# Kernel tuning notes

Hardware: AMD Instinct MI355X
Metric: run time of the kernel (lower is better)

## Reference

```python
import jax, jax.numpy as jnp
import numpy as np

P_DROP = 0.5

def _dropout(x, key):
    keep = jax.random.bernoulli(key, 1.0 - P_DROP, x.shape)
    return jnp.where(keep, x / (1.0 - P_DROP), 0.0)

def _sage_mean_agg(src, dst, feat_src, h_self, n_dst, key):
    # SAGEMeanAgg: dropout both inputs, copy_src gather, segment mean, add, relu
    k1, k2 = jax.random.split(key)
    feat_src = _dropout(feat_src, k1)
    h_self = _dropout(h_self, k2)
    msg = feat_src[src]                                   # [E, d] gather
    summ = jax.ops.segment_sum(msg, dst, num_segments=n_dst)
    deg = jax.ops.segment_sum(jnp.ones((dst.shape[0],), msg.dtype), dst, num_segments=n_dst)
    neigh = jnp.where(deg[:, None] > 0, summ / jnp.maximum(deg, 1.0)[:, None], 0.0)
    return jax.nn.relu(neigh + h_self)

def setup_inputs() -> dict:
    key = jax.random.key(0)
    ks = jax.random.split(key, 12)
    N_total, d_in, d_hid, d_out = 1200000, 128, 256, 47
    N0, N1, N2 = 10000, 100000, 1000000
    E0, E1 = 100000, 1000000
    return {
        "features": jax.random.normal(ks[0], (N_total, d_in), jnp.float32),
        "s0": jax.random.randint(ks[1], (N0,), 0, N_total),
        "s1": jax.random.randint(ks[2], (N1,), 0, N_total),
        "s2": jax.random.randint(ks[3], (N2,), 0, N_total),
        "src0": jax.random.randint(ks[4], (E0,), 0, N1),
        "dst0": jax.random.randint(ks[5], (E0,), 0, N0),
        "src1": jax.random.randint(ks[6], (E1,), 0, N2),
        "dst1": jax.random.randint(ks[7], (E1,), 0, N1),
        "W1": jax.random.normal(ks[8], (d_in, d_hid), jnp.float32) * 0.05,
        "b1": jnp.zeros((d_hid,), jnp.float32),
        "W2": jax.random.normal(ks[9], (d_hid, d_out), jnp.float32) * 0.05,
        "b2": jnp.zeros((d_out,), jnp.float32),
    }

def reference(features, s0, s1, s2, src0, dst0, src1, dst1, W1, b1, W2, b2):
    N0, N1 = s0.shape[0], s1.shape[0]
    dk = jax.random.split(jax.random.key(42), 3)
    h0 = features[s0]
    h1 = features[s1]
    h2 = features[s2]
    # layer 0 over 2 hops (shared linear W1)
    a0 = _sage_mean_agg(src0, dst0, h1, h0, N0, dk[0])
    n0 = a0 @ W1 + b1
    a1 = _sage_mean_agg(src1, dst1, h2, h1, N1, dk[1])
    n1 = a1 @ W1 + b1
    # layer 1 over 1 hop
    a = _sage_mean_agg(src0, dst0, n1, n0, N0, dk[2])
    return a @ W2 + b2
```

## Files before the change

kernel.cpp:

```cpp
#include <hip/hip_runtime.h>
#include <hip/hip_bf16.h>

typedef short v8s __attribute__((ext_vector_type(8)));
typedef float v4f __attribute__((ext_vector_type(4)));

__host__ __device__ __forceinline__ unsigned rotl32(unsigned x, int d) {
  return (x << d) | (x >> (32 - d));
}

__host__ __device__ __forceinline__ void threefry2x32(
    unsigned k0, unsigned k1, unsigned x0, unsigned x1,
    unsigned& o0, unsigned& o1) {
  unsigned ks2 = k0 ^ k1 ^ 0x1BD11BDAu;
  unsigned v0 = x0 + k0, v1 = x1 + k1;
#define TF_R(r) { v0 += v1; v1 = rotl32(v1, (r)); v1 ^= v0; }
  TF_R(13) TF_R(15) TF_R(26) TF_R(6)  v0 += k1;  v1 += ks2 + 1u;
  TF_R(17) TF_R(29) TF_R(16) TF_R(24) v0 += ks2; v1 += k0 + 2u;
  TF_R(13) TF_R(15) TF_R(26) TF_R(6)  v0 += k0;  v1 += k1 + 3u;
  TF_R(17) TF_R(29) TF_R(16) TF_R(24) v0 += k1;  v1 += ks2 + 4u;
  TF_R(13) TF_R(15) TF_R(26) TF_R(6)  v0 += ks2; v1 += k0 + 5u;
#undef TF_R
  o0 = v0; o1 = v1;
}

__device__ __forceinline__ float drop_scale(unsigned ka, unsigned kb,
                                            unsigned pos) {
  unsigned o0, o1;
  threefry2x32(ka, kb, 0u, pos, o0, o1);
  return ((o0 ^ o1) >> 31) ? 0.0f : 2.0f;
}

__device__ __forceinline__ float bf2f(unsigned short u) {
  unsigned x = ((unsigned)u) << 16;
  float f;
  __builtin_memcpy(&f, &x, 4);
  return f;
}
__device__ __forceinline__ unsigned short f2bf(float f) {
  __hip_bfloat16 h = __float2bfloat16(f);
  unsigned short u;
  __builtin_memcpy(&u, &h, 2);
  return u;
}

__global__ __launch_bounds__(256) void k_init(
    int* __restrict__ deg1, int n1, int* __restrict__ deg0, int n0,
    const float* __restrict__ W1, unsigned short* __restrict__ W1T,
    const float* __restrict__ W2, unsigned short* __restrict__ W2Th,
    unsigned short* __restrict__ W2Tl) {
  int i = blockIdx.x * 256 + threadIdx.x;
  if (i < n1) deg1[i] = 0;
  if (i < n0) deg0[i] = 0;
  if (i < 32768) {
    int n = i >> 7, k = i & 127;
    W1T[n * 128 + k] = f2bf(W1[k * 256 + n]);
  } else if (i < 32768 + 48 * 256) {
    int j = i - 32768;
    int n = j >> 8, k = j & 255;
    float w = (n < 47) ? W2[k * 47 + n] : 0.f;
    unsigned short hi = f2bf(w);
    float r = w - bf2f(hi);
    W2Th[n * 256 + k] = hi;
    W2Tl[n * 256 + k] = f2bf(r);
  }
}

__global__ __launch_bounds__(256) void k_countm(
    const int* __restrict__ dst1, int* __restrict__ deg1, int E1,
    const int* __restrict__ dst0, int* __restrict__ deg0, int E0) {
  int e = blockIdx.x * 256 + threadIdx.x;
  if (e < E1) {
    atomicAdd(&deg1[dst1[e]], 1);
  } else {
    int e0 = e - E1;
    if (e0 < E0) atomicAdd(&deg0[dst0[e0]], 1);
  }
}

__global__ __launch_bounds__(256) void k_scan1m(
    const int* __restrict__ d1, int* __restrict__ o1, int* __restrict__ b1,
    int n1, int B1,
    const int* __restrict__ d0, int* __restrict__ o0, int* __restrict__ b0,
    int n0) {
  __shared__ int ls[256];
  const int* d; int* o; int* bs; int n; int blk;
  if ((int)blockIdx.x < B1) {
    d = d1; o = o1; bs = b1; n = n1; blk = blockIdx.x;
  } else {
    d = d0; o = o0; bs = b0; n = n0; blk = blockIdx.x - B1;
  }
  int t = threadIdx.x;
  int base = blk * 1024 + t * 4;
  int v[4], s = 0;
#pragma unroll
  for (int q = 0; q < 4; ++q) {
    int i = base + q;
    v[q] = (i < n) ? d[i] : 0;
    s += v[q];
  }
  ls[t] = s;
  __syncthreads();
  for (int off = 1; off < 256; off <<= 1) {
    int x = (t >= off) ? ls[t - off] : 0;
    __syncthreads();
    ls[t] += x;
    __syncthreads();
  }
  int run = ls[t] - s;
  if (t == 255) bs[blk] = ls[255];
#pragma unroll
  for (int q = 0; q < 4; ++q) {
    int i = base + q;
    if (i < n) o[i] = run;
    run += v[q];
  }
}

__global__ __launch_bounds__(256) void k_scan23m(
    int* __restrict__ o1, int* __restrict__ w1, const int* __restrict__ bs1_,
    int n1, int B1,
    int* __restrict__ o0, int* __restrict__ w0, const int* __restrict__ bs0_,
    int n0) {
  __shared__ int ls[256];
  int* o; int* w; const int* bs; int n; int blk;
  if ((int)blockIdx.x < B1) {
    o = o1; w = w1; bs = bs1_; n = n1; blk = blockIdx.x;
  } else {
    o = o0; w = w0; bs = bs0_; n = n0; blk = blockIdx.x - B1;
  }
  int t = threadIdx.x;
  ls[t] = (t < blk) ? bs[t] : 0;
  __syncthreads();
#pragma unroll
  for (int off = 128; off > 0; off >>= 1) {
    if (t < off) ls[t] += ls[t + off];
    __syncthreads();
  }
  int add = ls[0];
  int base = blk * 1024 + t * 4;
#pragma unroll
  for (int q = 0; q < 4; ++q) {
    int i = base + q;
    if (i < n) {
      int v = o[i] + add;
      o[i] = v;
      if (i < n - 1) w[i] = v;
    }
  }
}

__global__ __launch_bounds__(256) void k_fillm(
    const int* __restrict__ src1, const int* __restrict__ dst1,
    const int* __restrict__ s2, int* __restrict__ woff1,
    int2* __restrict__ csr1, int E1,
    const int* __restrict__ src0, const int* __restrict__ dst0,
    const int* __restrict__ s1, int* __restrict__ woff0,
    int2* __restrict__ csr0, int E0) {
  int e = blockIdx.x * 256 + threadIdx.x;
  if (e < E1) {
    int d = dst1[e];
    int pos = atomicAdd(&woff1[d], 1);
    int r = src1[e];
    csr1[pos] = make_int2(r, s2[r]);
  } else {
    int e0 = e - E1;
    if (e0 < E0) {
      int d = dst0[e0];
      int pos = atomicAdd(&woff0[d], 1);
      int r = src0[e0];
      csr0[pos] = make_int2(r, s1[r]);
    }
  }
}

__global__ __launch_bounds__(256) void k_agg128m(
    const float* __restrict__ feats,
    const int* __restrict__ off1, const int2* __restrict__ csr1,
    const int* __restrict__ sel1,
    const int* __restrict__ off0, const int2* __restrict__ csr0,
    const int* __restrict__ sel0,
    unsigned short* __restrict__ outbf, int N1, int Ntot,
    unsigned k1fa, unsigned k1fb, unsigned k1ha, unsigned k1hb,
    unsigned k0fa, unsigned k0fb, unsigned k0ha, unsigned k0hb) {
  int wave = (blockIdx.x * 256 + threadIdx.x) >> 6;
  int lane = threadIdx.x & 63;
  if (wave >= Ntot) return;
  const int* off; const int2* csr; const int* sel;
  unsigned kfa, kfb, kha, khb; int w;
  if (wave < N1) {
    off = off1; csr = csr1; sel = sel1;
    kfa = k1fa; kfb = k1fb; kha = k1ha; khb = k1hb; w = wave;
  } else {
    off = off0; csr = csr0; sel = sel0;
    kfa = k0fa; kfb = k0fb; kha = k0ha; khb = k0hb; w = wave - N1;
  }
  int beg = off[w], end = off[w + 1];
  float acc0 = 0.f, acc1 = 0.f;
  for (int base = beg; base < end; base += 64) {
    int idx = base + lane;
    int2 rg = make_int2(0, 0);
    if (idx < end) rg = csr[idx];
    int r_l = rg.x, g_l = rg.y;
    int cnt = min(64, end - base);
    int b = 0;
    for (; b + 2 <= cnt; b += 2) {
      int ra = __shfl(r_l, b),     ga = __shfl(g_l, b);
      int rb = __shfl(r_l, b + 1), gb = __shfl(g_l, b + 1);
      float2 fa = *(const float2*)(feats + (size_t)ga * 128 + lane * 2);
      float2 fb = *(const float2*)(feats + (size_t)gb * 128 + lane * 2);
      unsigned pa = (unsigned)ra * 128u + (unsigned)(lane * 2);
      unsigned pb = (unsigned)rb * 128u + (unsigned)(lane * 2);
      acc0 += fa.x * drop_scale(kfa, kfb, pa);
      acc1 += fa.y * drop_scale(kfa, kfb, pa + 1);
      acc0 += fb.x * drop_scale(kfa, kfb, pb);
      acc1 += fb.y * drop_scale(kfa, kfb, pb + 1);
    }
    if (b < cnt) {
      int r = __shfl(r_l, b), g = __shfl(g_l, b);
      float2 f = *(const float2*)(feats + (size_t)g * 128 + lane * 2);
      unsigned p = (unsigned)r * 128u + (unsigned)(lane * 2);
      acc0 += f.x * drop_scale(kfa, kfb, p);
      acc1 += f.y * drop_scale(kfa, kfb, p + 1);
    }
  }
  float deg = (float)(end - beg);
  float inv = deg > 0.f ? 1.0f / deg : 0.f;
  float n0 = acc0 * inv, n1 = acc1 * inv;
  float2 sf = *(const float2*)(feats + (size_t)sel[w] * 128 + lane * 2);
  unsigned ps = (unsigned)w * 128u + (unsigned)(lane * 2);
  float v0 = n0 + sf.x * drop_scale(kha, khb, ps);
  float v1 = n1 + sf.y * drop_scale(kha, khb, ps + 1);
  v0 = v0 > 0.f ? v0 : 0.f;
  v1 = v1 > 0.f ? v1 : 0.f;
  ushort2 u;
  u.x = f2bf(v0);
  u.y = f2bf(v1);
  *(ushort2*)(outbf + (size_t)wave * 128 + lane * 2) = u;
}

__global__ __launch_bounds__(256) void k_agg256(
    const unsigned short* __restrict__ X, const int* __restrict__ off,
    const int2* __restrict__ csr, const unsigned short* __restrict__ self,
    unsigned short* __restrict__ outbf, int N,
    unsigned kfa, unsigned kfb, unsigned kha, unsigned khb) {
  int wid = (blockIdx.x * 256 + threadIdx.x) >> 6;
  int lane = threadIdx.x & 63;
  if (wid >= 2 * N) return;
  int w = wid >> 1;
  int c0 = ((wid & 1) << 7) + lane * 2;
  int beg = off[w], end = off[w + 1];
  float a0 = 0.f, a1 = 0.f;
  for (int base = beg; base < end; base += 64) {
    int idx = base + lane;
    int r_l = 0;
    if (idx < end) r_l = csr[idx].x;
    int cnt = min(64, end - base);
    int b = 0;
    for (; b + 2 <= cnt; b += 2) {
      int ra = __shfl(r_l, b), rb = __shfl(r_l, b + 1);
      unsigned rawa = *(const unsigned*)(X + (size_t)ra * 256 + c0);
      unsigned rawb = *(const unsigned*)(X + (size_t)rb * 256 + c0);
      unsigned pa = (unsigned)ra * 256u + (unsigned)c0;
      unsigned pb = (unsigned)rb * 256u + (unsigned)c0;
      a0 += bf2f((unsigned short)rawa) * drop_scale(kfa, kfb, pa);
      a1 += bf2f((unsigned short)(rawa >> 16)) * drop_scale(kfa, kfb, pa + 1);
      a0 += bf2f((unsigned short)rawb) * drop_scale(kfa, kfb, pb);
      a1 += bf2f((unsigned short)(rawb >> 16)) * drop_scale(kfa, kfb, pb + 1);
    }
    if (b < cnt) {
      int r = __shfl(r_l, b);
      unsigned raw = *(const unsigned*)(X + (size_t)r * 256 + c0);
      unsigned p = (unsigned)r * 256u + (unsigned)c0;
      a0 += bf2f((unsigned short)raw) * drop_scale(kfa, kfb, p);
      a1 += bf2f((unsigned short)(raw >> 16)) * drop_scale(kfa, kfb, p + 1);
    }
  }
  float deg = (float)(end - beg);
  float inv = deg > 0.f ? 1.0f / deg : 0.f;
  unsigned sraw = *(const unsigned*)(self + (size_t)w * 256 + c0);
  unsigned ps = (unsigned)w * 256u + (unsigned)c0;
  float v0 = a0 * inv + bf2f((unsigned short)sraw) * drop_scale(kha, khb, ps);
  float v1 = a1 * inv +
             bf2f((unsigned short)(sraw >> 16)) * drop_scale(kha, khb, ps + 1);
  v0 = v0 > 0.f ? v0 : 0.f;
  v1 = v1 > 0.f ? v1 : 0.f;
  ushort2 u;
  u.x = f2bf(v0);
  u.y = f2bf(v1);
  *(ushort2*)(outbf + (size_t)w * 256 + c0) = u;
}

__global__ __launch_bounds__(256) void k_gemm1(
    const unsigned short* __restrict__ A, const unsigned short* __restrict__ W1T,
    const float* __restrict__ bias, unsigned short* __restrict__ C, int M) {
  __shared__ unsigned short As[128 * 72];
  __shared__ unsigned short Bs[128 * 72];
  const int t = threadIdx.x;
  const int r0 = blockIdx.x * 128, n0 = blockIdx.y * 128;
  const int wv = t >> 6, lane = t & 63;
  const int mb = (wv >> 1) * 64, nb = (wv & 1) * 64;
  const int qm = lane & 15, quad = lane >> 4;
  v4f acc[4][4];
#pragma unroll
  for (int i = 0; i < 4; ++i)
#pragma unroll
    for (int j = 0; j < 4; ++j) acc[i][j] = (v4f){0.f, 0.f, 0.f, 0.f};

  for (int kt = 0; kt < 128; kt += 64) {
#pragma unroll
    for (int it = 0; it < 4; ++it) {
      int i = t + it * 256;
      int r = i >> 3, c = i & 7;
      uint4 v = make_uint4(0, 0, 0, 0);
      int gr = r0 + r;
      if (gr < M) v = ((const uint4*)A)[(size_t)gr * 16 + (kt >> 3) + c];
      *(uint4*)&As[r * 72 + c * 8] = v;
    }
#pragma unroll
    for (int it = 0; it < 4; ++it) {
      int i = t + it * 256;
      int n = i >> 3, c = i & 7;
      uint4 v = ((const uint4*)W1T)[(size_t)(n0 + n) * 16 + (kt >> 3) + c];
      *(uint4*)&Bs[n * 72 + c * 8] = v;
    }
    __syncthreads();
#pragma unroll
    for (int kk = 0; kk < 64; kk += 32) {
      v8s af[4], bf_[4];
#pragma unroll
      for (int i = 0; i < 4; ++i)
        af[i] = *(const v8s*)&As[(mb + i * 16 + qm) * 72 + kk + quad * 8];
#pragma unroll
      for (int j = 0; j < 4; ++j)
        bf_[j] = *(const v8s*)&Bs[(nb + j * 16 + qm) * 72 + kk + quad * 8];
#pragma unroll
      for (int i = 0; i < 4; ++i)
#pragma unroll
        for (int j = 0; j < 4; ++j)
          acc[i][j] = __builtin_amdgcn_mfma_f32_16x16x32_bf16(
              af[i], bf_[j], acc[i][j], 0, 0, 0);
    }
    __syncthreads();
  }
  const int col_base = n0 + nb + qm;
  float bj[4];
#pragma unroll
  for (int j = 0; j < 4; ++j) bj[j] = bias[col_base + j * 16];
#pragma unroll
  for (int i = 0; i < 4; ++i) {
    int row = r0 + mb + i * 16 + quad * 4;
#pragma unroll
    for (int reg = 0; reg < 4; ++reg) {
      int rr = row + reg;
      if (rr < M) {
#pragma unroll
        for (int j = 0; j < 4; ++j)
          C[(size_t)rr * 256 + col_base + j * 16] = f2bf(acc[i][j][reg] + bj[j]);
      }
    }
  }
}

__global__ __launch_bounds__(256) void k_gemm2(
    const unsigned short* __restrict__ A, const unsigned short* __restrict__ Bh,
    const unsigned short* __restrict__ Bl, const float* __restrict__ b2,
    float* __restrict__ out, int M) {
  const int t = threadIdx.x;
  const int wv = t >> 6, lane = t & 63;
  const int qm = lane & 15, quad = lane >> 4;
  const int rw = blockIdx.x * 64 + wv * 16;
  v4f acc[3];
#pragma unroll
  for (int j = 0; j < 3; ++j) acc[j] = (v4f){0.f, 0.f, 0.f, 0.f};
  int arow = rw + qm;
  if (arow >= M) arow = M - 1;
  const unsigned short* Ar = A + (size_t)arow * 256;
#pragma unroll
  for (int kk = 0; kk < 256; kk += 32) {
    v8s af = *(const v8s*)&Ar[kk + quad * 8];
#pragma unroll
    for (int j = 0; j < 3; ++j) {
      v8s bh = *(const v8s*)&Bh[(size_t)(j * 16 + qm) * 256 + kk + quad * 8];
      v8s bl = *(const v8s*)&Bl[(size_t)(j * 16 + qm) * 256 + kk + quad * 8];
      acc[j] = __builtin_amdgcn_mfma_f32_16x16x32_bf16(af, bh, acc[j], 0, 0, 0);
      acc[j] = __builtin_amdgcn_mfma_f32_16x16x32_bf16(af, bl, acc[j], 0, 0, 0);
    }
  }
#pragma unroll
  for (int j = 0; j < 3; ++j) {
    int col = j * 16 + qm;
    if (col >= 47) continue;
    float bb = b2[col];
#pragma unroll
    for (int reg = 0; reg < 4; ++reg) {
      int row = rw + quad * 4 + reg;
      if (row < M) out[(size_t)row * 47 + col] = acc[j][reg] + bb;
    }
  }
}

static inline size_t alignup(size_t x) { return (x + 255) & ~(size_t)255; }

extern "C" void kernel_launch(void* const* d_in, const int* in_sizes, int n_in,
                              void* d_out, int out_size, void* d_ws,
                              size_t ws_size, hipStream_t stream) {
  const float* features = (const float*)d_in[0];
  const int* s0   = (const int*)d_in[1];
  const int* s1   = (const int*)d_in[2];
  const int* s2   = (const int*)d_in[3];
  const int* src0 = (const int*)d_in[4];
  const int* dst0 = (const int*)d_in[5];
  const int* src1 = (const int*)d_in[6];
  const int* dst1 = (const int*)d_in[7];
  const float* W1 = (const float*)d_in[8];
  const float* b1 = (const float*)d_in[9];
  const float* W2 = (const float*)d_in[10];
  const float* b2 = (const float*)d_in[11];
  float* out = (float*)d_out;

  const int N0 = in_sizes[1], N1 = in_sizes[2];
  const int E0 = in_sizes[4], E1 = in_sizes[6];
  const int Ntot = N1 + N0;
  const int Etot = E1 + E0;

  unsigned dk[3][2], kfs[3][2], khs[3][2];
  for (int i = 0; i < 3; ++i)
    threefry2x32(0u, 42u, 0u, (unsigned)i, dk[i][0], dk[i][1]);
  for (int i = 0; i < 3; ++i) {
    threefry2x32(dk[i][0], dk[i][1], 0u, 0u, kfs[i][0], kfs[i][1]);
    threefry2x32(dk[i][0], dk[i][1], 0u, 1u, khs[i][0], khs[i][1]);
  }

  char* p = (char*)d_ws;
  auto take = [&](size_t bytes) {
    char* r = p;
    p += alignup(bytes);
    return r;
  };
  unsigned short* a_all = (unsigned short*)take((size_t)Ntot * 128 * 2);
  unsigned short* n_all = (unsigned short*)take((size_t)Ntot * 256 * 2);
  unsigned short* a2bf  = (unsigned short*)take((size_t)N0 * 256 * 2);
  unsigned short* w1t   = (unsigned short*)take(256 * 128 * 2);
  unsigned short* w2th  = (unsigned short*)take(48 * 256 * 2);
  unsigned short* w2tl  = (unsigned short*)take(48 * 256 * 2);
  int* off1  = (int*)take((size_t)(N1 + 2) * 4);
  int* woff1 = (int*)take((size_t)N1 * 4);
  int* deg1  = (int*)take((size_t)(N1 + 2) * 4);
  int* off0  = (int*)take((size_t)(N0 + 2) * 4);
  int* woff0 = (int*)take((size_t)N0 * 4);
  int* deg0  = (int*)take((size_t)(N0 + 2) * 4);
  int* bs1   = (int*)take(1024 * 4);
  int* bs0   = (int*)take(1024 * 4);
  int2* csr1 = (int2*)take((size_t)E1 * 8);
  int2* csr0 = (int2*)take((size_t)E0 * 8);

  {
    int span = N1 + 2;
    if (N0 + 2 > span) span = N0 + 2;
    if (32768 + 48 * 256 > span) span = 32768 + 48 * 256;
    k_init<<<(span + 255) / 256, 256, 0, stream>>>(deg1, N1 + 2, deg0, N0 + 2,
                                                   W1, w1t, W2, w2th, w2tl);
  }
  k_countm<<<(Etot + 255) / 256, 256, 0, stream>>>(dst1, deg1, E1, dst0, deg0,
                                                   E0);

  const int n1s = N1 + 1, B1 = (n1s + 1023) / 1024;
  const int n0s = N0 + 1, B0 = (n0s + 1023) / 1024;
  k_scan1m<<<B1 + B0, 256, 0, stream>>>(deg1, off1, bs1, n1s, B1,
                                        deg0, off0, bs0, n0s);
  k_scan23m<<<B1 + B0, 256, 0, stream>>>(off1, woff1, bs1, n1s, B1,
                                         off0, woff0, bs0, n0s);

  k_fillm<<<(Etot + 255) / 256, 256, 0, stream>>>(
      src1, dst1, s2, woff1, csr1, E1,
      src0, dst0, s1, woff0, csr0, E0);

  k_agg128m<<<(Ntot + 3) / 4, 256, 0, stream>>>(
      features, off1, csr1, s1, off0, csr0, s0, a_all, N1, Ntot,
      kfs[1][0], kfs[1][1], khs[1][0], khs[1][1],
      kfs[0][0], kfs[0][1], khs[0][0], khs[0][1]);
  {
    dim3 g((Ntot + 127) / 128, 2);
    k_gemm1<<<g, 256, 0, stream>>>(a_all, w1t, b1, n_all, Ntot);
  }

  k_agg256<<<(2 * N0 + 3) / 4, 256, 0, stream>>>(
      n_all, off0, csr0, n_all + (size_t)N1 * 256, a2bf, N0,
      kfs[2][0], kfs[2][1], khs[2][0], khs[2][1]);
  k_gemm2<<<(N0 + 63) / 64, 256, 0, stream>>>(a2bf, w2th, w2tl, b2, out, N0);
}
```

Before: 1.157 ms.

## Fuse two-pass scan into single-pass with cross-block flags; widen agg256 parallelism

Merges the two prefix-scan kernels into one that publishes per-block totals through flag words and spin-waits on earlier blocks, which removes one launch and one reread of the offsets. k_agg256 now uses four waves per destination row, each covering one bf16 column, instead of two waves covering two columns each, to raise parallelism on the small layer. k_agg128 precomputes scaled row offsets before the shuffles to save per-edge integer math. The spin-wait assumes every earlier block gets scheduled; with about 100 blocks that holds on this GPU. The agg256 change trades 4-byte loads for 2-byte loads.

```diff
diff --git a/kernel.cpp b/kernel.cpp
--- a/kernel.cpp
+++ b/kernel.cpp
@@ -45,12 +45,14 @@
 
 __global__ __launch_bounds__(256) void k_init(
     int* __restrict__ deg1, int n1, int* __restrict__ deg0, int n0,
+    unsigned* __restrict__ fl1, unsigned* __restrict__ fl0,
     const float* __restrict__ W1, unsigned short* __restrict__ W1T,
     const float* __restrict__ W2, unsigned short* __restrict__ W2Th,
     unsigned short* __restrict__ W2Tl) {
   int i = blockIdx.x * 256 + threadIdx.x;
   if (i < n1) deg1[i] = 0;
   if (i < n0) deg0[i] = 0;
+  if (i < 1024) { fl1[i] = 0u; fl0[i] = 0u; }
   if (i < 32768) {
     int n = i >> 7, k = i & 127;
     W1T[n * 128 + k] = f2bf(W1[k * 256 + n]);
@@ -77,17 +79,17 @@
   }
 }
 
-__global__ __launch_bounds__(256) void k_scan1m(
-    const int* __restrict__ d1, int* __restrict__ o1, int* __restrict__ b1,
-    int n1, int B1,
-    const int* __restrict__ d0, int* __restrict__ o0, int* __restrict__ b0,
-    int n0) {
+__global__ __launch_bounds__(256) void k_scanlb(
+    const int* __restrict__ d1, int* __restrict__ o1, int* __restrict__ w1,
+    unsigned* __restrict__ fl1, int n1, int B1,
+    const int* __restrict__ d0, int* __restrict__ o0, int* __restrict__ w0,
+    unsigned* __restrict__ fl0, int n0) {
   __shared__ int ls[256];
-  const int* d; int* o; int* bs; int n; int blk;
+  const int* d; int* o; int* w; unsigned* fl; int n; int blk;
   if ((int)blockIdx.x < B1) {
-    d = d1; o = o1; bs = b1; n = n1; blk = blockIdx.x;
+    d = d1; o = o1; w = w1; fl = fl1; n = n1; blk = blockIdx.x;
   } else {
-    d = d0; o = o0; bs = b0; n = n0; blk = blockIdx.x - B1;
+    d = d0; o = o0; w = w0; fl = fl0; n = n0; blk = blockIdx.x - B1;
   }
   int t = threadIdx.x;
   int base = blk * 1024 + t * 4;
@@ -107,29 +109,20 @@
     __syncthreads();
   }
   int run = ls[t] - s;
-  if (t == 255) bs[blk] = ls[255];
-#pragma unroll
-  for (int q = 0; q < 4; ++q) {
-    int i = base + q;
-    if (i < n) o[i] = run;
-    run += v[q];
-  }
-}
-
-__global__ __launch_bounds__(256) void k_scan23m(
-    int* __restrict__ o1, int* __restrict__ w1, const int* __restrict__ bs1_,
-    int n1, int B1,
-    int* __restrict__ o0, int* __restrict__ w0, const int* __restrict__ bs0_,
-    int n0) {
-  __shared__ int ls[256];
-  int* o; int* w; const int* bs; int n; int blk;
-  if ((int)blockIdx.x < B1) {
-    o = o1; w = w1; bs = bs1_; n = n1; blk = blockIdx.x;
-  } else {
-    o = o0; w = w0; bs = bs0_; n = n0; blk = blockIdx.x - B1;
-  }
-  int t = threadIdx.x;
-  ls[t] = (t < blk) ? bs[t] : 0;
+  int tot = ls[255];
+  if (t == 0)
+    __hip_atomic_store(&fl[blk], 0x80000000u | (unsigned)tot,
+                       __ATOMIC_RELEASE, __HIP_MEMORY_SCOPE_AGENT);
+  unsigned mine = 0;
+  if (t < blk) {
+    unsigned x;
+    do {
+      x = __hip_atomic_load(&fl[t], __ATOMIC_ACQUIRE, __HIP_MEMORY_SCOPE_AGENT);
+    } while (!(x >> 31));
+    mine = x & 0x7fffffffu;
+  }
+  __syncthreads();
+  ls[t] = (int)mine;
   __syncthreads();
 #pragma unroll
   for (int off = 128; off > 0; off >>= 1) {
@@ -137,15 +130,15 @@
     __syncthreads();
   }
   int add = ls[0];
-  int base = blk * 1024 + t * 4;
 #pragma unroll
   for (int q = 0; q < 4; ++q) {
     int i = base + q;
     if (i < n) {
-      int v = o[i] + add;
-      o[i] = v;
-      if (i < n - 1) w[i] = v;
-    }
+      int vv = run + add;
+      o[i] = vv;
+      if (i < n - 1) w[i] = vv;
+    }
+    run += v[q];
   }
 }
 
@@ -194,40 +187,39 @@
     off = off0; csr = csr0; sel = sel0;
     kfa = k0fa; kfb = k0fb; kha = k0ha; khb = k0hb; w = wave - N1;
   }
+  const unsigned ll2 = (unsigned)(lane * 2);
   int beg = off[w], end = off[w + 1];
   float acc0 = 0.f, acc1 = 0.f;
   for (int base = beg; base < end; base += 64) {
     int idx = base + lane;
     int2 rg = make_int2(0, 0);
     if (idx < end) rg = csr[idx];
-    int r_l = rg.x, g_l = rg.y;
+    unsigned pr_l = (unsigned)rg.x * 128u;
+    unsigned pg_l = (unsigned)rg.y * 128u;
     int cnt = min(64, end - base);
     int b = 0;
     for (; b + 2 <= cnt; b += 2) {
-      int ra = __shfl(r_l, b),     ga = __shfl(g_l, b);
-      int rb = __shfl(r_l, b + 1), gb = __shfl(g_l, b + 1);
-      float2 fa = *(const float2*)(feats + (size_t)ga * 128 + lane * 2);
-      float2 fb = *(const float2*)(feats + (size_t)gb * 128 + lane * 2);
-      unsigned pa = (unsigned)ra * 128u + (unsigned)(lane * 2);
-      unsigned pb = (unsigned)rb * 128u + (unsigned)(lane * 2);
-      acc0 += fa.x * drop_scale(kfa, kfb, pa);
-      acc1 += fa.y * drop_scale(kfa, kfb, pa + 1);
-      acc0 += fb.x * drop_scale(kfa, kfb, pb);
-      acc1 += fb.y * drop_scale(kfa, kfb, pb + 1);
+      unsigned pra = __shfl(pr_l, b),     pga = __shfl(pg_l, b);
+      unsigned prb = __shfl(pr_l, b + 1), pgb = __shfl(pg_l, b + 1);
+      float2 fa = *(const float2*)(feats + (size_t)pga + ll2);
+      float2 fb = *(const float2*)(feats + (size_t)pgb + ll2);
+      acc0 += fa.x * drop_scale(kfa, kfb, pra + ll2);
+      acc1 += fa.y * drop_scale(kfa, kfb, pra + ll2 + 1);
+      acc0 += fb.x * drop_scale(kfa, kfb, prb + ll2);
+      acc1 += fb.y * drop_scale(kfa, kfb, prb + ll2 + 1);
     }
     if (b < cnt) {
-      int r = __shfl(r_l, b), g = __shfl(g_l, b);
-      float2 f = *(const float2*)(feats + (size_t)g * 128 + lane * 2);
-      unsigned p = (unsigned)r * 128u + (unsigned)(lane * 2);
-      acc0 += f.x * drop_scale(kfa, kfb, p);
-      acc1 += f.y * drop_scale(kfa, kfb, p + 1);
+      unsigned pr = __shfl(pr_l, b), pg = __shfl(pg_l, b);
+      float2 f = *(const float2*)(feats + (size_t)pg + ll2);
+      acc0 += f.x * drop_scale(kfa, kfb, pr + ll2);
+      acc1 += f.y * drop_scale(kfa, kfb, pr + ll2 + 1);
     }
   }
   float deg = (float)(end - beg);
   float inv = deg > 0.f ? 1.0f / deg : 0.f;
   float n0 = acc0 * inv, n1 = acc1 * inv;
-  float2 sf = *(const float2*)(feats + (size_t)sel[w] * 128 + lane * 2);
-  unsigned ps = (unsigned)w * 128u + (unsigned)(lane * 2);
+  float2 sf = *(const float2*)(feats + (size_t)sel[w] * 128 + ll2);
+  unsigned ps = (unsigned)w * 128u + ll2;
   float v0 = n0 + sf.x * drop_scale(kha, khb, ps);
   float v1 = n1 + sf.y * drop_scale(kha, khb, ps + 1);
   v0 = v0 > 0.f ? v0 : 0.f;
@@ -235,7 +227,7 @@
   ushort2 u;
   u.x = f2bf(v0);
   u.y = f2bf(v1);
-  *(ushort2*)(outbf + (size_t)wave * 128 + lane * 2) = u;
+  *(ushort2*)(outbf + (size_t)wave * 128 + ll2) = u;
 }
 
 __global__ __launch_bounds__(256) void k_agg256(
@@ -245,49 +237,36 @@
     unsigned kfa, unsigned kfb, unsigned kha, unsigned khb) {
   int wid = (blockIdx.x * 256 + threadIdx.x) >> 6;
   int lane = threadIdx.x & 63;
-  if (wid >= 2 * N) return;
-  int w = wid >> 1;
-  int c0 = ((wid & 1) << 7) + lane * 2;
+  if (wid >= 4 * N) return;
+  int w = wid >> 2;
+  unsigned c0 = (unsigned)(((wid & 3) << 6) + lane);
   int beg = off[w], end = off[w + 1];
-  float a0 = 0.f, a1 = 0.f;
+  float a0 = 0.f;
   for (int base = beg; base < end; base += 64) {
     int idx = base + lane;
-    int r_l = 0;
-    if (idx < end) r_l = csr[idx].x;
+    unsigned p_l = 0;
+    if (idx < end) p_l = (unsigned)csr[idx].x * 256u;
     int cnt = min(64, end - base);
     int b = 0;
     for (; b + 2 <= cnt; b += 2) {
-      int ra = __shfl(r_l, b), rb = __shfl(r_l, b + 1);
-      unsigned rawa = *(const unsigned*)(X + (size_t)ra * 256 + c0);
-      unsigned rawb = *(const unsigned*)(X + (size_t)rb * 256 + c0);
-      unsigned pa = (unsigned)ra * 256u + (unsigned)c0;
-      unsigned pb = (unsigned)rb * 256u + (unsigned)c0;
-      a0 += bf2f((unsigned short)rawa) * drop_scale(kfa, kfb, pa);
-      a1 += bf2f((unsigned short)(rawa >> 16)) * drop_scale(kfa, kfb, pa + 1);
-      a0 += bf2f((unsigned short)rawb) * drop_scale(kfa, kfb, pb);
-      a1 += bf2f((unsigned short)(rawb >> 16)) * drop_scale(kfa, kfb, pb + 1);
+      unsigned pa = __shfl(p_l, b), pb = __shfl(p_l, b + 1);
+      float fa = bf2f(X[(size_t)pa + c0]);
+      float fb = bf2f(X[(size_t)pb + c0]);
+      a0 += fa * drop_scale(kfa, kfb, pa + c0);
+      a0 += fb * drop_scale(kfa, kfb, pb + c0);
     }
     if (b < cnt) {
-      int r = __shfl(r_l, b);
-      unsigned raw = *(const unsigned*)(X + (size_t)r * 256 + c0);
-      unsigned p = (unsigned)r * 256u + (unsigned)c0;
-      a0 += bf2f((unsigned short)raw) * drop_scale(kfa, kfb, p);
-      a1 += bf2f((unsigned short)(raw >> 16)) * drop_scale(kfa, kfb, p + 1);
+      unsigned p = __shfl(p_l, b);
+      a0 += bf2f(X[(size_t)p + c0]) * drop_scale(kfa, kfb, p + c0);
     }
   }
   float deg = (float)(end - beg);
   float inv = deg > 0.f ? 1.0f / deg : 0.f;
-  unsigned sraw = *(const unsigned*)(self + (size_t)w * 256 + c0);
-  unsigned ps = (unsigned)w * 256u + (unsigned)c0;
-  float v0 = a0 * inv + bf2f((unsigned short)sraw) * drop_scale(kha, khb, ps);
-  float v1 = a1 * inv +
-             bf2f((unsigned short)(sraw >> 16)) * drop_scale(kha, khb, ps + 1);
-  v0 = v0 > 0.f ? v0 : 0.f;
-  v1 = v1 > 0.f ? v1 : 0.f;
-  ushort2 u;
-  u.x = f2bf(v0);
-  u.y = f2bf(v1);
-  *(ushort2*)(outbf + (size_t)w * 256 + c0) = u;
+  unsigned ps = (unsigned)w * 256u + c0;
+  float v = a0 * inv +
+            bf2f(self[(size_t)w * 256 + c0]) * drop_scale(kha, khb, ps);
+  v = v > 0.f ? v : 0.f;
+  outbf[(size_t)w * 256 + c0] = f2bf(v);
 }
 
 __global__ __launch_bounds__(256) void k_gemm1(
@@ -449,8 +428,8 @@
   int* off0  = (int*)take((size_t)(N0 + 2) * 4);
   int* woff0 = (int*)take((size_t)N0 * 4);
   int* deg0  = (int*)take((size_t)(N0 + 2) * 4);
-  int* bs1   = (int*)take(1024 * 4);
-  int* bs0   = (int*)take(1024 * 4);
+  unsigned* fl1 = (unsigned*)take(1024 * 4);
+  unsigned* fl0 = (unsigned*)take(1024 * 4);
   int2* csr1 = (int2*)take((size_t)E1 * 8);
   int2* csr0 = (int2*)take((size_t)E0 * 8);
 
@@ -458,18 +437,16 @@
     int span = N1 + 2;
     if (N0 + 2 > span) span = N0 + 2;
     if (32768 + 48 * 256 > span) span = 32768 + 48 * 256;
-    k_init<<<(span + 255) / 256, 256, 0, stream>>>(deg1, N1 + 2, deg0, N0 + 2,
-                                                   W1, w1t, W2, w2th, w2tl);
+    k_init<<<(span + 255) / 256, 256, 0, stream>>>(
+        deg1, N1 + 2, deg0, N0 + 2, fl1, fl0, W1, w1t, W2, w2th, w2tl);
   }
   k_countm<<<(Etot + 255) / 256, 256, 0, stream>>>(dst1, deg1, E1, dst0, deg0,
                                                    E0);
 
   const int n1s = N1 + 1, B1 = (n1s + 1023) / 1024;
   const int n0s = N0 + 1, B0 = (n0s + 1023) / 1024;
-  k_scan1m<<<B1 + B0, 256, 0, stream>>>(deg1, off1, bs1, n1s, B1,
-                                        deg0, off0, bs0, n0s);
-  k_scan23m<<<B1 + B0, 256, 0, stream>>>(off1, woff1, bs1, n1s, B1,
-                                         off0, woff0, bs0, n0s);
+  k_scanlb<<<B1 + B0, 256, 0, stream>>>(deg1, off1, woff1, fl1, n1s, B1,
+                                        deg0, off0, woff0, fl0, n0s);
 
   k_fillm<<<(Etot + 255) / 256, 256, 0, stream>>>(
       src1, dst1, s2, woff1, csr1, E1,
@@ -484,7 +461,7 @@
     k_gemm1<<<g, 256, 0, stream>>>(a_all, w1t, b1, n_all, Ntot);
   }
 
-  k_agg256<<<(2 * N0 + 3) / 4, 256, 0, stream>>>(
+  k_agg256<<<(4 * N0 + 3) / 4, 256, 0, stream>>>(
       n_all, off0, csr0, n_all + (size_t)N1 * 256, a2bf, N0,
       kfs[2][0], kfs[2][1], khs[2][0], khs[2][1]);
   k_gemm2<<<(N0 + 63) / 64, 256, 0, stream>>>(a2bf, w2th, w2tl, b2, out, N0);
```

New measurement: 1.152 ms. About the same (-0.4%).
